# Kernel optimization log

Hardware: AMD Instinct MI355X
Metric: run time of the kernel (lower is better)

Reference implementation:

```python
import jax, jax.numpy as jnp
import numpy as np

# Sizes
N = 4096        # nodes
E = 32768       # edges
NEF = 128       # n_edge_features
HID = 128       # hidden_features
MUL0 = 64       # multiplicity of 0e irreps
MUL1 = 16       # multiplicity of 1o irreps
DIM = MUL0 + 3 * MUL1  # 112
# e3nn FullyConnectedTensorProduct('64x0e+16x1o', '1x0e+1x1o', '64x0e+16x1o')
# instruction order (i_in1, i_in2, i_out): (0,0,0),(0,1,1),(1,0,1),(1,1,0)
WN_A = MUL0 * MUL0   # 0e x 0e -> 0e : 4096
WN_B = MUL0 * MUL1   # 0e x 1o -> 1o : 1024
WN_C = MUL1 * MUL1   # 1o x 0e -> 1o : 256
WN_D = MUL1 * MUL0   # 1o x 1o -> 0e : 1024
WNUM = WN_A + WN_B + WN_C + WN_D  # 6400
# path normalization (irrep_normalization='component', path_normalization='element'):
# alpha = dim(ir_out) / sum_{paths into same output}(mul1*mul2)
N0 = float(np.sqrt(1.0 / (MUL0 + MUL1)))       # scalar output: 1/sqrt(80)
N1 = float(np.sqrt(3.0 / (MUL0 + MUL1)))       # vector output: sqrt(3/80)
INV_SQRT3 = float(1.0 / np.sqrt(3.0))          # wigner-3j factor for l=1 paths


def setup_inputs() -> dict:
    key = jax.random.key(0)
    ks = jax.random.split(key, 8)
    node_attr = jax.random.normal(ks[0], (N, DIM), jnp.float32)
    edge_index = jax.random.randint(ks[1], (2, E), 0, N)
    edge_attr = jax.random.normal(ks[2], (E, NEF), jnp.float32)
    edge_sh = jax.random.normal(ks[3], (E, 4), jnp.float32)
    global_graph_embedding = jax.random.normal(ks[4], (8, 1024), jnp.float32)
    ptr = jnp.sort(jax.random.randint(ks[5], (9,), 0, N))
    W1 = jax.random.normal(ks[6], (NEF, HID), jnp.float32) / np.sqrt(NEF)
    b1 = jnp.zeros((HID,), jnp.float32)
    W2 = jax.random.normal(ks[7], (HID, WNUM), jnp.float32) / np.sqrt(HID)
    b2 = jnp.zeros((WNUM,), jnp.float32)
    return dict(node_attr=node_attr, edge_index=edge_index, edge_attr=edge_attr,
                edge_sh=edge_sh, global_graph_embedding=global_graph_embedding,
                ptr=ptr, W1=W1, b1=b1, W2=W2, b2=b2)


def _tp_conv(node_attr, src, dst, edge_attr, edge_sh, W1, b1, W2, b2):
    # edge MLP -> per-edge tensor-product weights
    h = jax.nn.relu(edge_attr @ W1 + b1)
    w = h @ W2 + b2                                   # (E, 6400)
    # gather and split gathered node features into irreps
    x = node_attr[dst]                                # (E, 112)
    s = x[:, :MUL0]                                   # (E, 64) scalars 0e
    v = x[:, MUL0:].reshape(-1, MUL1, 3)              # (E, 16, 3) vectors 1o
    sh0 = edge_sh[:, :1]                              # (E, 1)
    sh1 = edge_sh[:, 1:]                              # (E, 3)
    i = 0
    wA = w[:, i:i + WN_A].reshape(-1, MUL0, MUL0); i += WN_A
    wB = w[:, i:i + WN_B].reshape(-1, MUL0, MUL1); i += WN_B
    wC = w[:, i:i + WN_C].reshape(-1, MUL1, MUL1); i += WN_C
    wD = w[:, i:i + WN_D].reshape(-1, MUL1, MUL0); i += WN_D
    # scalar output channel: 0e*0e->0e  and  1o.1o->0e (dot product CG)
    out0 = N0 * (jnp.einsum('euw,eu->ew', wA, s) * sh0
                 + INV_SQRT3 * jnp.einsum('euw,eui,ei->ew', wD, v, sh1))
    # vector output channel: 0e*1o->1o  and  1o*0e->1o
    out1 = N1 * (INV_SQRT3 * jnp.einsum('euw,eu,ei->ewi', wB, s, sh1)
                 + INV_SQRT3 * jnp.einsum('euw,eui->ewi', wC, v) * sh0[:, :, None])
    tp = jnp.concatenate([out0, out1.reshape(-1, 3 * MUL1)], axis=-1)  # (E, 112)
    # scatter-mean over edge_src (torch_scatter 'mean': empty segments -> 0)
    sums = jax.ops.segment_sum(tp, src, num_segments=N)
    cnt = jax.ops.segment_sum(jnp.ones((tp.shape[0],), tp.dtype), src, num_segments=N)
    return sums / jnp.maximum(cnt, 1.0)[:, None]


def reference(node_attr, edge_index, edge_attr, edge_sh, global_graph_embedding, ptr, W1, b1, W2, b2):
    src, dst = edge_index[0], edge_index[1]
    out = _tp_conv(node_attr, src, dst, edge_attr, edge_sh, W1, b1, W2, b2)
    # add_in=False -> global branch skipped; residual: in/out dims equal so F.pad is identity
    return out + node_attr
```

## Files before the change

kernel.cpp:

```cpp
#include <hip/hip_runtime.h>

typedef unsigned short u16;
typedef __bf16 bf8 __attribute__((ext_vector_type(8)));
typedef float f4 __attribute__((ext_vector_type(4)));

#define E_EDGES 32768
#define N_NODES 4096
#define N0_CONST 0.1118033988749895f
#define INV_SQRT3_CONST 0.5773502691896258f

__device__ __forceinline__ u16 f2bf(float f) {
    unsigned u = __float_as_uint(f);
    u += 0x7FFFu + ((u >> 16) & 1u);
    return (u16)(u >> 16);
}

__global__ __launch_bounds__(256) void k_prep(const float* __restrict__ W2, const float* __restrict__ W1,
                                              const int* __restrict__ edge_index,
                                              u16* __restrict__ w2s, u16* __restrict__ w1t,
                                              int* __restrict__ deg) {
    int b = blockIdx.x;
    int tid = threadIdx.x;
    if (b < 400) {
        int ks = tid >> 6, l = tid & 63;
        int el = l & 15, q4 = l >> 4;
        int c = b * 16 + el;
        u16 tmp[8];
#pragma unroll
        for (int j = 0; j < 8; j++) {
            int k = ks * 32 + q4 * 8 + j;
            tmp[j] = f2bf(W2[(size_t)k * 6400 + c]);
        }
        *(uint4*)(w2s + b * 2048 + ks * 512 + l * 8) = *(uint4*)tmp;
    } else if (b < 416) {
        int t = (b - 400) * 256 + tid;
#pragma unroll
        for (int i = 0; i < 4; i++) {
            int idx = t * 4 + i;
            int c = idx >> 7, k = idx & 127;
            w1t[idx] = f2bf(W1[k * 128 + c]);
        }
    } else {
        int t = (b - 416) * 256 + tid;
        atomicAdd(&deg[edge_index[t]], 1);
    }
}

__global__ void k_scan(const int* __restrict__ deg, int* __restrict__ ptr, int* __restrict__ cursor) {
    int t = threadIdx.x;
    int base = t * 64;
    int s = 0;
    for (int i = 0; i < 64; i++) s += deg[base + i];
    int x = s;
#pragma unroll
    for (int d = 1; d < 64; d <<= 1) {
        int y = __shfl_up(x, d, 64);
        if (t >= d) x += y;
    }
    int run = x - s;
    for (int i = 0; i < 64; i++) {
        ptr[base + i] = run;
        cursor[base + i] = run;
        run += deg[base + i];
    }
    if (t == 63) ptr[4096] = run;
}

__global__ __launch_bounds__(256) void k_h(const float* __restrict__ ea,
                                           const u16* __restrict__ w1t,
                                           const float* __restrict__ b1,
                                           const int* __restrict__ edge_index,
                                           int* __restrict__ cursor,
                                           int* __restrict__ eids,
                                           u16* __restrict__ h) {
    __shared__ alignas(16) u16 ea_s[64][128];
    int tid = threadIdx.x;
    int e0 = blockIdx.x * 64;
    if (tid < 64) {
        int ge = e0 + tid;
        int s = edge_index[ge];
        int pos = atomicAdd(&cursor[s], 1);
        eids[pos] = ge;
    }
    {
        int e = tid >> 2, q = tid & 3;
        const float4* src = (const float4*)(ea + (size_t)(e0 + e) * 128 + q * 32);
#pragma unroll
        for (int i = 0; i < 8; i++) {
            float4 f = src[i];
            int c = q * 32 + i * 4;
            ea_s[e][c + 0] = f2bf(f.x); ea_s[e][c + 1] = f2bf(f.y);
            ea_s[e][c + 2] = f2bf(f.z); ea_s[e][c + 3] = f2bf(f.w);
        }
    }
    __syncthreads();
    int lane = tid & 63, wave = tid >> 6;
    int el = lane & 15, q4 = lane >> 4;
    f4 acc[4][2];
#pragma unroll
    for (int m = 0; m < 4; m++)
#pragma unroll
        for (int nt = 0; nt < 2; nt++) acc[m][nt] = (f4){0.f, 0.f, 0.f, 0.f};
#pragma unroll
    for (int ks = 0; ks < 4; ks++) {
        bf8 a[4], b[2];
#pragma unroll
        for (int m = 0; m < 4; m++) a[m] = *(const bf8*)&ea_s[m * 16 + el][ks * 32 + q4 * 8];
#pragma unroll
        for (int nt = 0; nt < 2; nt++) {
            int n = wave * 32 + nt * 16 + el;
            b[nt] = *(const bf8*)(w1t + n * 128 + ks * 32 + q4 * 8);
        }
#pragma unroll
        for (int m = 0; m < 4; m++)
#pragma unroll
            for (int nt = 0; nt < 2; nt++)
                acc[m][nt] = __builtin_amdgcn_mfma_f32_16x16x32_bf16(a[m], b[nt], acc[m][nt], 0, 0, 0);
    }
#pragma unroll
    for (int m = 0; m < 4; m++)
#pragma unroll
        for (int nt = 0; nt < 2; nt++) {
            int n = wave * 32 + nt * 16 + el;
            float bias = b1[n];
#pragma unroll
            for (int r = 0; r < 4; r++) {
                int e = e0 + m * 16 + q4 * 4 + r;
                float v = fmaxf(acc[m][nt][r] + bias, 0.f);
                h[(size_t)e * 128 + n] = f2bf(v);
            }
        }
}

__global__ __launch_bounds__(256, 2) void k_main(const u16* __restrict__ w2s,
                                                 const u16* __restrict__ hgl,
                                                 const float* __restrict__ b2,
                                                 const float* __restrict__ node_attr,
                                                 const int* __restrict__ edge_index,
                                                 const float* __restrict__ edge_sh,
                                                 float* __restrict__ tp) {
    __shared__ alignas(16) union {
        u16 h[64][136];
        struct { float bcB[64][17]; float bcC[3][64][17]; } bc;
    } ovl;
    __shared__ float sT[64][66];
    __shared__ float vT[3][16][66];
    __shared__ float pT[16][66];
    __shared__ float sh0_s[64];
    __shared__ float sh1_s[3][64];
    __shared__ int dst_s[64];

    int tid = threadIdx.x;
    int e0 = blockIdx.x * 64;
    int lane = tid & 63, wave = tid >> 6;
    int el = lane & 15, q4 = lane >> 4;

    bf8 a0[4], a1[4];
    float4 bb0, bb1;
    auto loadA = [&](int i, bf8 (&a)[4], float4& bb) {
        int g = (i < 20) ? 64 + i : (i < 84 ? i - 20 : i);
        int pn = 4 * g + wave;
        const u16* gp = w2s + (size_t)pn * 2048 + lane * 8;
        a[0] = *(const bf8*)(gp);
        a[1] = *(const bf8*)(gp + 512);
        a[2] = *(const bf8*)(gp + 1024);
        a[3] = *(const bf8*)(gp + 1536);
        bb = *(const float4*)(b2 + pn * 16 + q4 * 4);
    };
    loadA(0, a0, bb0);

    if (tid < 64) {
        int ge = e0 + tid;
        dst_s[tid] = edge_index[E_EDGES + ge];
        float4 sh = *(const float4*)(edge_sh + (size_t)ge * 4);
        sh0_s[tid] = sh.x; sh1_s[0][tid] = sh.y; sh1_s[1][tid] = sh.z; sh1_s[2][tid] = sh.w;
    }
    __syncthreads();

    {
        int e = tid >> 2, q = tid & 3;
        int dst = dst_s[e];
        const float* xp = node_attr + (size_t)dst * 112;
#pragma unroll
        for (int i = 0; i < 4; i++) {
            float4 f = *(const float4*)(xp + q * 16 + i * 4);
            int u = q * 16 + i * 4;
            sT[u + 0][e] = f.x; sT[u + 1][e] = f.y; sT[u + 2][e] = f.z; sT[u + 3][e] = f.w;
        }
        float vv[12];
#pragma unroll
        for (int i = 0; i < 3; i++) {
            float4 f = *(const float4*)(xp + 64 + q * 12 + i * 4);
            vv[i * 4 + 0] = f.x; vv[i * 4 + 1] = f.y; vv[i * 4 + 2] = f.z; vv[i * 4 + 3] = f.w;
        }
        float s1x = sh1_s[0][e], s1y = sh1_s[1][e], s1z = sh1_s[2][e];
#pragma unroll
        for (int u = 0; u < 4; u++) {
            float xa = vv[u * 3 + 0], xb = vv[u * 3 + 1], xc = vv[u * 3 + 2];
            int uu = q * 4 + u;
            vT[0][uu][e] = xa; vT[1][uu][e] = xb; vT[2][uu][e] = xc;
            pT[uu][e] = INV_SQRT3_CONST * (xa * s1x + xb * s1y + xc * s1z);
        }
        const uint4* hsrc = (const uint4*)(hgl + (size_t)(e0 + e) * 128) + q * 4;
        uint4* hdst = (uint4*)(&ovl.h[e][q * 32]);
#pragma unroll
        for (int i = 0; i < 4; i++) hdst[i] = hsrc[i];
    }
    __syncthreads();

    bf8 hbf[4][4];
#pragma unroll
    for (int nt = 0; nt < 4; nt++)
#pragma unroll
        for (int ks = 0; ks < 4; ks++)
            hbf[nt][ks] = *(const bf8*)&ovl.h[nt * 16 + el][ks * 32 + q4 * 8];
    float sh0n4[4];
#pragma unroll
    for (int nt = 0; nt < 4; nt++) sh0n4[nt] = sh0_s[nt * 16 + el];
    __syncthreads();

    for (int idx = tid; idx < 4352; idx += 256) ((float*)&ovl.bc)[idx] = 0.f;
    __syncthreads();

    auto mfmaG = [&](const bf8 (&a)[4], const float4& bb, f4 (&wf)[4]) {
#pragma unroll
        for (int nt = 0; nt < 4; nt++) wf[nt] = (f4){bb.x, bb.y, bb.z, bb.w};
#pragma unroll
        for (int ks = 0; ks < 4; ks++)
#pragma unroll
            for (int nt = 0; nt < 4; nt++)
                wf[nt] = __builtin_amdgcn_mfma_f32_16x16x32_bf16(a[ks], hbf[nt][ks], wf[nt], 0, 0, 0);
    };

#define STEP(INXT, ACUR, BBCUR, ANXT, BBNXT, CON) \
    { if ((INXT) < 100) loadA((INXT), ANXT, BBNXT); mfmaG(ACUR, BBCUR, wf); CON; }

    f4 wf[4];

    {
        f4 accBn[4];
#pragma unroll
        for (int nt = 0; nt < 4; nt++) accBn[nt] = (f4){0.f, 0.f, 0.f, 0.f};
        auto conB = [&](int ib) {
            int u = 4 * ib + wave;
#pragma unroll
            for (int nt = 0; nt < 4; nt++) {
                float f = sT[u][nt * 16 + el];
                accBn[nt] += f * wf[nt];
            }
        };
        for (int ii = 0; ii < 16; ii += 2) {
            STEP(ii + 1, a0, bb0, a1, bb1, conB(ii));
            STEP(ii + 2, a1, bb1, a0, bb0, conB(ii + 1));
        }
#pragma unroll
        for (int nt = 0; nt < 4; nt++)
#pragma unroll
            for (int r = 0; r < 4; r++)
                atomicAdd(&ovl.bc.bcB[nt * 16 + el][q4 * 4 + r], accBn[nt][r]);
    }

    {
        f4 accCn[3][4];
#pragma unroll
        for (int i3 = 0; i3 < 3; i3++)
#pragma unroll
            for (int nt = 0; nt < 4; nt++) accCn[i3][nt] = (f4){0.f, 0.f, 0.f, 0.f};
        auto conC = [&](int ic) {
            int u = 4 * ic + wave;
#pragma unroll
            for (int nt = 0; nt < 4; nt++) {
#pragma unroll
                for (int i3 = 0; i3 < 3; i3++) {
                    float f = vT[i3][u][nt * 16 + el];
                    accCn[i3][nt] += f * wf[nt];
                }
            }
        };
        for (int ii = 0; ii < 4; ii += 2) {
            STEP(16 + ii + 1, a0, bb0, a1, bb1, conC(ii));
            STEP(16 + ii + 2, a1, bb1, a0, bb0, conC(ii + 1));
        }
#pragma unroll
        for (int i3 = 0; i3 < 3; i3++)
#pragma unroll
            for (int nt = 0; nt < 4; nt++)
#pragma unroll
                for (int r = 0; r < 4; r++)
                    atomicAdd(&ovl.bc.bcC[i3][nt * 16 + el][q4 * 4 + r], accCn[i3][nt][r]);
    }

    f4 acc0n[4];
#pragma unroll
    for (int nt = 0; nt < 4; nt++) acc0n[nt] = (f4){0.f, 0.f, 0.f, 0.f};
    {
        auto conA = [&](int ia) {
#pragma unroll
            for (int nt = 0; nt < 4; nt++) {
                float f = sh0n4[nt] * sT[ia][nt * 16 + el];
                acc0n[nt] += f * wf[nt];
            }
        };
        for (int ii = 0; ii < 64; ii += 2) {
            STEP(20 + ii + 1, a0, bb0, a1, bb1, conA(ii));
            STEP(20 + ii + 2, a1, bb1, a0, bb0, conA(ii + 1));
        }
        auto conD = [&](int id_) {
#pragma unroll
            for (int nt = 0; nt < 4; nt++) {
                float f = pT[id_][nt * 16 + el];
                acc0n[nt] += f * wf[nt];
            }
        };
        for (int ii = 0; ii < 16; ii += 2) {
            STEP(84 + ii + 1, a0, bb0, a1, bb1, conD(ii));
            STEP(84 + ii + 2, a1, bb1, a0, bb0, conD(ii + 1));
        }
    }
#undef STEP

    __syncthreads();

#pragma unroll
    for (int nt = 0; nt < 4; nt++)
#pragma unroll
        for (int r = 0; r < 4; r++)
            sT[nt * 16 + el][wave * 16 + q4 * 4 + r] = N0_CONST * acc0n[nt][r];
    {
        float* vflat = (float*)vT;
        for (int idx = tid; idx < 3072; idx += 256) {
            int e = idx / 48;
            int rem = idx - e * 48;
            int w = rem / 3;
            int i3 = rem - w * 3;
            vflat[idx] = N0_CONST * (ovl.bc.bcB[e][w] * sh1_s[i3][e] + ovl.bc.bcC[i3][e][w] * sh0_s[e]);
        }
    }
    __syncthreads();

    {
        const float* vflat = (const float*)vT;
        float* tpe = tp + (size_t)e0 * 112;
        for (int idx = tid; idx < 64 * 112; idx += 256) {
            int e = idx / 112;
            int c = idx - e * 112;
            float val = (c < 64) ? sT[e][c] : vflat[e * 48 + (c - 64)];
            __builtin_nontemporal_store(val, &tpe[idx]);
        }
    }
}

__global__ __launch_bounds__(128) void k_red(const float* __restrict__ tp,
                                             const int* __restrict__ ptr,
                                             const int* __restrict__ eids,
                                             const float* __restrict__ node_attr,
                                             float* __restrict__ out) {
    int n = blockIdx.x;
    int c = threadIdx.x;
    if (c >= 112) return;
    int a = ptr[n], b = ptr[n + 1];
    float s = 0.f;
    for (int i = a; i < b; i++) {
        int e = eids[i];
        s += tp[(size_t)e * 112 + c];
    }
    float d = fmaxf((float)(b - a), 1.f);
    out[n * 112 + c] = s / d + node_attr[n * 112 + c];
}

extern "C" void kernel_launch(void* const* d_in, const int* in_sizes, int n_in,
                              void* d_out, int out_size, void* d_ws, size_t ws_size,
                              hipStream_t stream) {
    const float* node_attr  = (const float*)d_in[0];
    const int*   edge_index = (const int*)d_in[1];
    const float* edge_attr  = (const float*)d_in[2];
    const float* edge_sh    = (const float*)d_in[3];
    const float* W1         = (const float*)d_in[6];
    const float* b1         = (const float*)d_in[7];
    const float* W2         = (const float*)d_in[8];
    const float* b2         = (const float*)d_in[9];
    float* out = (float*)d_out;

    char* ws = (char*)d_ws;
    u16*   w2s    = (u16*)ws;
    u16*   w1t    = (u16*)(ws + 1638400);
    u16*   hgl    = (u16*)(ws + 1671168);
    float* tp     = (float*)(ws + 10059776);
    int*   deg    = (int*)(ws + 24739840);
    int*   ptr    = (int*)(ws + 24756224);
    int*   cursor = (int*)(ws + 24772624);
    int*   eids   = (int*)(ws + 24789024);

    hipMemsetAsync(deg, 0, 16384, stream);
    k_prep<<<544, 256, 0, stream>>>(W2, W1, edge_index, w2s, w1t, deg);
    k_scan<<<1, 64, 0, stream>>>(deg, ptr, cursor);
    k_h<<<512, 256, 0, stream>>>(edge_attr, w1t, b1, edge_index, cursor, eids, hgl);
    k_main<<<512, 256, 0, stream>>>(w2s, hgl, b2, node_attr, edge_index, edge_sh, tp);
    k_red<<<4096, 128, 0, stream>>>(tp, ptr, eids, node_attr, out);
}
```

Before: 196.3 us.

## Split k_main MFMA K-dimension across two wave halves with 512-thread blocks

Doubles k_main blocks to 512 threads and splits the 128-wide hidden K dimension between two groups of four waves, so each wave holds half the A and B fragments and issues half the MFMAs per step. Partial sums are combined through shared-memory atomics (now issued per step for the C path) and a second-phase add into sT for the scalar outputs. The aim is more waves per CU to hide W2 load latency and lower register pressure. The cost is extra LDS atomics, an extra barrier, and duplicated contraction work, since both halves run the FMA contraction on their own partial weights.

```diff
diff --git a/kernel.cpp b/kernel.cpp
--- a/kernel.cpp
+++ b/kernel.cpp
@@ -132,7 +132,7 @@
         }
 }
 
-__global__ __launch_bounds__(256, 2) void k_main(const u16* __restrict__ w2s,
+__global__ __launch_bounds__(512, 4) void k_main(const u16* __restrict__ w2s,
                                                  const u16* __restrict__ hgl,
                                                  const float* __restrict__ b2,
                                                  const float* __restrict__ node_attr,
@@ -153,19 +153,19 @@
     int tid = threadIdx.x;
     int e0 = blockIdx.x * 64;
     int lane = tid & 63, wave = tid >> 6;
+    int tl = wave & 3, half = wave >> 2;
     int el = lane & 15, q4 = lane >> 4;
 
-    bf8 a0[4], a1[4];
+    bf8 a0[2], a1[2];
     float4 bb0, bb1;
-    auto loadA = [&](int i, bf8 (&a)[4], float4& bb) {
+    auto loadA = [&](int i, bf8 (&a)[2], float4& bb) {
         int g = (i < 20) ? 64 + i : (i < 84 ? i - 20 : i);
-        int pn = 4 * g + wave;
-        const u16* gp = w2s + (size_t)pn * 2048 + lane * 8;
+        int pn = 4 * g + tl;
+        const u16* gp = w2s + (size_t)pn * 2048 + half * 1024 + lane * 8;
         a[0] = *(const bf8*)(gp);
         a[1] = *(const bf8*)(gp + 512);
-        a[2] = *(const bf8*)(gp + 1024);
-        a[3] = *(const bf8*)(gp + 1536);
-        bb = *(const float4*)(b2 + pn * 16 + q4 * 4);
+        bb = (half == 0) ? *(const float4*)(b2 + pn * 16 + q4 * 4)
+                         : (float4){0.f, 0.f, 0.f, 0.f};
     };
     loadA(0, a0, bb0);
 
@@ -177,7 +177,7 @@
     }
     __syncthreads();
 
-    {
+    if (tid < 256) {
         int e = tid >> 2, q = tid & 3;
         int dst = dst_s[e];
         const float* xp = node_attr + (size_t)dst * 112;
@@ -208,25 +208,25 @@
     }
     __syncthreads();
 
-    bf8 hbf[4][4];
+    bf8 hbf[4][2];
 #pragma unroll
     for (int nt = 0; nt < 4; nt++)
 #pragma unroll
-        for (int ks = 0; ks < 4; ks++)
-            hbf[nt][ks] = *(const bf8*)&ovl.h[nt * 16 + el][ks * 32 + q4 * 8];
+        for (int ks = 0; ks < 2; ks++)
+            hbf[nt][ks] = *(const bf8*)&ovl.h[nt * 16 + el][half * 64 + ks * 32 + q4 * 8];
     float sh0n4[4];
 #pragma unroll
     for (int nt = 0; nt < 4; nt++) sh0n4[nt] = sh0_s[nt * 16 + el];
     __syncthreads();
 
-    for (int idx = tid; idx < 4352; idx += 256) ((float*)&ovl.bc)[idx] = 0.f;
-    __syncthreads();
-
-    auto mfmaG = [&](const bf8 (&a)[4], const float4& bb, f4 (&wf)[4]) {
+    for (int idx = tid; idx < 4352; idx += 512) ((float*)&ovl.bc)[idx] = 0.f;
+    __syncthreads();
+
+    auto mfmaG = [&](const bf8 (&a)[2], const float4& bb, f4 (&wf)[4]) {
 #pragma unroll
         for (int nt = 0; nt < 4; nt++) wf[nt] = (f4){bb.x, bb.y, bb.z, bb.w};
 #pragma unroll
-        for (int ks = 0; ks < 4; ks++)
+        for (int ks = 0; ks < 2; ks++)
 #pragma unroll
             for (int nt = 0; nt < 4; nt++)
                 wf[nt] = __builtin_amdgcn_mfma_f32_16x16x32_bf16(a[ks], hbf[nt][ks], wf[nt], 0, 0, 0);
@@ -242,7 +242,7 @@
 #pragma unroll
         for (int nt = 0; nt < 4; nt++) accBn[nt] = (f4){0.f, 0.f, 0.f, 0.f};
         auto conB = [&](int ib) {
-            int u = 4 * ib + wave;
+            int u = 4 * ib + tl;
 #pragma unroll
             for (int nt = 0; nt < 4; nt++) {
                 float f = sT[u][nt * 16 + el];
@@ -261,19 +261,17 @@
     }
 
     {
-        f4 accCn[3][4];
-#pragma unroll
-        for (int i3 = 0; i3 < 3; i3++)
-#pragma unroll
-            for (int nt = 0; nt < 4; nt++) accCn[i3][nt] = (f4){0.f, 0.f, 0.f, 0.f};
         auto conC = [&](int ic) {
-            int u = 4 * ic + wave;
+            int u = 4 * ic + tl;
 #pragma unroll
             for (int nt = 0; nt < 4; nt++) {
 #pragma unroll
                 for (int i3 = 0; i3 < 3; i3++) {
                     float f = vT[i3][u][nt * 16 + el];
-                    accCn[i3][nt] += f * wf[nt];
+                    f4 t = f * wf[nt];
+#pragma unroll
+                    for (int r = 0; r < 4; r++)
+                        atomicAdd(&ovl.bc.bcC[i3][nt * 16 + el][q4 * 4 + r], t[r]);
                 }
             }
         };
@@ -281,13 +279,6 @@
             STEP(16 + ii + 1, a0, bb0, a1, bb1, conC(ii));
             STEP(16 + ii + 2, a1, bb1, a0, bb0, conC(ii + 1));
         }
-#pragma unroll
-        for (int i3 = 0; i3 < 3; i3++)
-#pragma unroll
-            for (int nt = 0; nt < 4; nt++)
-#pragma unroll
-                for (int r = 0; r < 4; r++)
-                    atomicAdd(&ovl.bc.bcC[i3][nt * 16 + el][q4 * 4 + r], accCn[i3][nt][r]);
     }
 
     f4 acc0n[4];
@@ -321,14 +312,16 @@
 
     __syncthreads();
 
-#pragma unroll
-    for (int nt = 0; nt < 4; nt++)
-#pragma unroll
-        for (int r = 0; r < 4; r++)
-            sT[nt * 16 + el][wave * 16 + q4 * 4 + r] = N0_CONST * acc0n[nt][r];
+    if (half == 0) {
+#pragma unroll
+        for (int nt = 0; nt < 4; nt++)
+#pragma unroll
+            for (int r = 0; r < 4; r++)
+                sT[nt * 16 + el][tl * 16 + q4 * 4 + r] = N0_CONST * acc0n[nt][r];
+    }
     {
         float* vflat = (float*)vT;
-        for (int idx = tid; idx < 3072; idx += 256) {
+        for (int idx = tid; idx < 3072; idx += 512) {
             int e = idx / 48;
             int rem = idx - e * 48;
             int w = rem / 3;
@@ -337,11 +330,19 @@
         }
     }
     __syncthreads();
+    if (half == 1) {
+#pragma unroll
+        for (int nt = 0; nt < 4; nt++)
+#pragma unroll
+            for (int r = 0; r < 4; r++)
+                sT[nt * 16 + el][tl * 16 + q4 * 4 + r] += N0_CONST * acc0n[nt][r];
+    }
+    __syncthreads();
 
     {
         const float* vflat = (const float*)vT;
         float* tpe = tp + (size_t)e0 * 112;
-        for (int idx = tid; idx < 64 * 112; idx += 256) {
+        for (int idx = tid; idx < 64 * 112; idx += 512) {
             int e = idx / 112;
             int c = idx - e * 112;
             float val = (c < 64) ? sT[e][c] : vflat[e * 48 + (c - 64)];
@@ -395,6 +396,6 @@
     k_prep<<<544, 256, 0, stream>>>(W2, W1, edge_index, w2s, w1t, deg);
     k_scan<<<1, 64, 0, stream>>>(deg, ptr, cursor);
     k_h<<<512, 256, 0, stream>>>(edge_attr, w1t, b1, edge_index, cursor, eids, hgl);
-    k_main<<<512, 256, 0, stream>>>(w2s, hgl, b2, node_attr, edge_index, edge_sh, tp);
+    k_main<<<512, 512, 0, stream>>>(w2s, hgl, b2, node_attr, edge_index, edge_sh, tp);
     k_red<<<4096, 128, 0, stream>>>(tp, ptr, eids, node_attr, out);
 }
```

New measurement: 560.5 us. 2.86x slower.

## Halve edges per k_main block to raise occupancy and stage W2 transpose via LDS

Applied to the files above, without the earlier changes.

k_main now handles 32 edges per block instead of 64. This shrinks the register accumulators and shared-memory tiles, doubles the grid to 1024 blocks, and raises the launch-bounds occupancy hint from 2 to 4 blocks per CU. In exchange, each block streams the full set of W2 A-fragments for half as many edges, so W2 weight traffic per edge doubles. Separately, k_prep reads W2 rows coalesced into a padded shared tile before converting to bf16, replacing strided global reads.

```diff
diff --git a/kernel.cpp b/kernel.cpp
--- a/kernel.cpp
+++ b/kernel.cpp
@@ -22,15 +22,23 @@
     int b = blockIdx.x;
     int tid = threadIdx.x;
     if (b < 400) {
+        __shared__ float w2l[128][17];
+        {
+            int k = tid >> 1, c8 = (tid & 1) * 8;
+            const float* src = W2 + (size_t)k * 6400 + b * 16 + c8;
+            float tmpf[8];
+#pragma unroll
+            for (int j = 0; j < 8; j++) tmpf[j] = src[j];
+#pragma unroll
+            for (int j = 0; j < 8; j++) w2l[k][c8 + j] = tmpf[j];
+        }
+        __syncthreads();
         int ks = tid >> 6, l = tid & 63;
         int el = l & 15, q4 = l >> 4;
-        int c = b * 16 + el;
         u16 tmp[8];
 #pragma unroll
-        for (int j = 0; j < 8; j++) {
-            int k = ks * 32 + q4 * 8 + j;
-            tmp[j] = f2bf(W2[(size_t)k * 6400 + c]);
-        }
+        for (int j = 0; j < 8; j++)
+            tmp[j] = f2bf(w2l[ks * 32 + q4 * 8 + j][el]);
         *(uint4*)(w2s + b * 2048 + ks * 512 + l * 8) = *(uint4*)tmp;
     } else if (b < 416) {
         int t = (b - 400) * 256 + tid;
@@ -132,7 +140,7 @@
         }
 }
 
-__global__ __launch_bounds__(256, 2) void k_main(const u16* __restrict__ w2s,
+__global__ __launch_bounds__(256, 4) void k_main(const u16* __restrict__ w2s,
                                                  const u16* __restrict__ hgl,
                                                  const float* __restrict__ b2,
                                                  const float* __restrict__ node_attr,
@@ -140,18 +148,18 @@
                                                  const float* __restrict__ edge_sh,
                                                  float* __restrict__ tp) {
     __shared__ alignas(16) union {
-        u16 h[64][136];
-        struct { float bcB[64][17]; float bcC[3][64][17]; } bc;
+        u16 h[32][136];
+        struct { float bcB[32][17]; float bcC[3][32][17]; } bc;
     } ovl;
-    __shared__ float sT[64][66];
-    __shared__ float vT[3][16][66];
-    __shared__ float pT[16][66];
-    __shared__ float sh0_s[64];
-    __shared__ float sh1_s[3][64];
-    __shared__ int dst_s[64];
+    __shared__ float sT[64][34];
+    __shared__ float vT[3][16][34];
+    __shared__ float pT[16][34];
+    __shared__ float sh0_s[32];
+    __shared__ float sh1_s[3][32];
+    __shared__ int dst_s[32];
 
     int tid = threadIdx.x;
-    int e0 = blockIdx.x * 64;
+    int e0 = blockIdx.x * 32;
     int lane = tid & 63, wave = tid >> 6;
     int el = lane & 15, q4 = lane >> 4;
 
@@ -169,7 +177,7 @@
     };
     loadA(0, a0, bb0);
 
-    if (tid < 64) {
+    if (tid < 32) {
         int ge = e0 + tid;
         dst_s[tid] = edge_index[E_EDGES + ge];
         float4 sh = *(const float4*)(edge_sh + (size_t)ge * 4);
@@ -178,73 +186,77 @@
     __syncthreads();
 
     {
-        int e = tid >> 2, q = tid & 3;
-        int dst = dst_s[e];
-        const float* xp = node_attr + (size_t)dst * 112;
-#pragma unroll
-        for (int i = 0; i < 4; i++) {
-            float4 f = *(const float4*)(xp + q * 16 + i * 4);
-            int u = q * 16 + i * 4;
-            sT[u + 0][e] = f.x; sT[u + 1][e] = f.y; sT[u + 2][e] = f.z; sT[u + 3][e] = f.w;
-        }
-        float vv[12];
-#pragma unroll
-        for (int i = 0; i < 3; i++) {
-            float4 f = *(const float4*)(xp + 64 + q * 12 + i * 4);
-            vv[i * 4 + 0] = f.x; vv[i * 4 + 1] = f.y; vv[i * 4 + 2] = f.z; vv[i * 4 + 3] = f.w;
-        }
-        float s1x = sh1_s[0][e], s1y = sh1_s[1][e], s1z = sh1_s[2][e];
-#pragma unroll
-        for (int u = 0; u < 4; u++) {
-            float xa = vv[u * 3 + 0], xb = vv[u * 3 + 1], xc = vv[u * 3 + 2];
-            int uu = q * 4 + u;
-            vT[0][uu][e] = xa; vT[1][uu][e] = xb; vT[2][uu][e] = xc;
-            pT[uu][e] = INV_SQRT3_CONST * (xa * s1x + xb * s1y + xc * s1z);
-        }
-        const uint4* hsrc = (const uint4*)(hgl + (size_t)(e0 + e) * 128) + q * 4;
-        uint4* hdst = (uint4*)(&ovl.h[e][q * 32]);
-#pragma unroll
-        for (int i = 0; i < 4; i++) hdst[i] = hsrc[i];
-    }
-    __syncthreads();
-
-    bf8 hbf[4][4];
-#pragma unroll
-    for (int nt = 0; nt < 4; nt++)
+        int e = tid >> 3, q = tid & 7;
+        if (q < 4) {
+            int dst = dst_s[e];
+            const float* xp = node_attr + (size_t)dst * 112;
+#pragma unroll
+            for (int i = 0; i < 4; i++) {
+                float4 f = *(const float4*)(xp + q * 16 + i * 4);
+                int u = q * 16 + i * 4;
+                sT[u + 0][e] = f.x; sT[u + 1][e] = f.y; sT[u + 2][e] = f.z; sT[u + 3][e] = f.w;
+            }
+            float vv[12];
+#pragma unroll
+            for (int i = 0; i < 3; i++) {
+                float4 f = *(const float4*)(xp + 64 + q * 12 + i * 4);
+                vv[i * 4 + 0] = f.x; vv[i * 4 + 1] = f.y; vv[i * 4 + 2] = f.z; vv[i * 4 + 3] = f.w;
+            }
+            float s1x = sh1_s[0][e], s1y = sh1_s[1][e], s1z = sh1_s[2][e];
+#pragma unroll
+            for (int u = 0; u < 4; u++) {
+                float xa = vv[u * 3 + 0], xb = vv[u * 3 + 1], xc = vv[u * 3 + 2];
+                int uu = q * 4 + u;
+                vT[0][uu][e] = xa; vT[1][uu][e] = xb; vT[2][uu][e] = xc;
+                pT[uu][e] = INV_SQRT3_CONST * (xa * s1x + xb * s1y + xc * s1z);
+            }
+        } else {
+            int qq = q - 4;
+            const uint4* hsrc = (const uint4*)(hgl + (size_t)(e0 + e) * 128) + qq * 4;
+            uint4* hdst = (uint4*)(&ovl.h[e][qq * 32]);
+#pragma unroll
+            for (int i = 0; i < 4; i++) hdst[i] = hsrc[i];
+        }
+    }
+    __syncthreads();
+
+    bf8 hbf[2][4];
+#pragma unroll
+    for (int nt = 0; nt < 2; nt++)
 #pragma unroll
         for (int ks = 0; ks < 4; ks++)
             hbf[nt][ks] = *(const bf8*)&ovl.h[nt * 16 + el][ks * 32 + q4 * 8];
-    float sh0n4[4];
-#pragma unroll
-    for (int nt = 0; nt < 4; nt++) sh0n4[nt] = sh0_s[nt * 16 + el];
-    __syncthreads();
-
-    for (int idx = tid; idx < 4352; idx += 256) ((float*)&ovl.bc)[idx] = 0.f;
-    __syncthreads();
-
-    auto mfmaG = [&](const bf8 (&a)[4], const float4& bb, f4 (&wf)[4]) {
-#pragma unroll
-        for (int nt = 0; nt < 4; nt++) wf[nt] = (f4){bb.x, bb.y, bb.z, bb.w};
+    float sh0n2[2];
+#pragma unroll
+    for (int nt = 0; nt < 2; nt++) sh0n2[nt] = sh0_s[nt * 16 + el];
+    __syncthreads();
+
+    for (int idx = tid; idx < 2176; idx += 256) ((float*)&ovl.bc)[idx] = 0.f;
+    __syncthreads();
+
+    auto mfmaG = [&](const bf8 (&a)[4], const float4& bb, f4 (&wf)[2]) {
+#pragma unroll
+        for (int nt = 0; nt < 2; nt++) wf[nt] = (f4){bb.x, bb.y, bb.z, bb.w};
 #pragma unroll
         for (int ks = 0; ks < 4; ks++)
 #pragma unroll
-            for (int nt = 0; nt < 4; nt++)
+            for (int nt = 0; nt < 2; nt++)
                 wf[nt] = __builtin_amdgcn_mfma_f32_16x16x32_bf16(a[ks], hbf[nt][ks], wf[nt], 0, 0, 0);
     };
 
 #define STEP(INXT, ACUR, BBCUR, ANXT, BBNXT, CON) \
     { if ((INXT) < 100) loadA((INXT), ANXT, BBNXT); mfmaG(ACUR, BBCUR, wf); CON; }
 
-    f4 wf[4];
-
-    {
-        f4 accBn[4];
-#pragma unroll
-        for (int nt = 0; nt < 4; nt++) accBn[nt] = (f4){0.f, 0.f, 0.f, 0.f};
+    f4 wf[2];
+
+    {
+        f4 accBn[2];
+#pragma unroll
+        for (int nt = 0; nt < 2; nt++) accBn[nt] = (f4){0.f, 0.f, 0.f, 0.f};
         auto conB = [&](int ib) {
             int u = 4 * ib + wave;
 #pragma unroll
-            for (int nt = 0; nt < 4; nt++) {
+            for (int nt = 0; nt < 2; nt++) {
                 float f = sT[u][nt * 16 + el];
                 accBn[nt] += f * wf[nt];
             }
@@ -254,22 +266,22 @@
             STEP(ii + 2, a1, bb1, a0, bb0, conB(ii + 1));
         }
 #pragma unroll
-        for (int nt = 0; nt < 4; nt++)
+        for (int nt = 0; nt < 2; nt++)
 #pragma unroll
             for (int r = 0; r < 4; r++)
                 atomicAdd(&ovl.bc.bcB[nt * 16 + el][q4 * 4 + r], accBn[nt][r]);
     }
 
     {
-        f4 accCn[3][4];
+        f4 accCn[3][2];
 #pragma unroll
         for (int i3 = 0; i3 < 3; i3++)
 #pragma unroll
-            for (int nt = 0; nt < 4; nt++) accCn[i3][nt] = (f4){0.f, 0.f, 0.f, 0.f};
+            for (int nt = 0; nt < 2; nt++) accCn[i3][nt] = (f4){0.f, 0.f, 0.f, 0.f};
         auto conC = [&](int ic) {
             int u = 4 * ic + wave;
 #pragma unroll
-            for (int nt = 0; nt < 4; nt++) {
+            for (int nt = 0; nt < 2; nt++) {
 #pragma unroll
                 for (int i3 = 0; i3 < 3; i3++) {
                     float f = vT[i3][u][nt * 16 + el];
@@ -284,20 +296,20 @@
 #pragma unroll
         for (int i3 = 0; i3 < 3; i3++)
 #pragma unroll
-            for (int nt = 0; nt < 4; nt++)
+            for (int nt = 0; nt < 2; nt++)
 #pragma unroll
                 for (int r = 0; r < 4; r++)
                     atomicAdd(&ovl.bc.bcC[i3][nt * 16 + el][q4 * 4 + r], accCn[i3][nt][r]);
     }
 
-    f4 acc0n[4];
-#pragma unroll
-    for (int nt = 0; nt < 4; nt++) acc0n[nt] = (f4){0.f, 0.f, 0.f, 0.f};
+    f4 acc0n[2];
+#pragma unroll
+    for (int nt = 0; nt < 2; nt++) acc0n[nt] = (f4){0.f, 0.f, 0.f, 0.f};
     {
         auto conA = [&](int ia) {
 #pragma unroll
-            for (int nt = 0; nt < 4; nt++) {
-                float f = sh0n4[nt] * sT[ia][nt * 16 + el];
+            for (int nt = 0; nt < 2; nt++) {
+                float f = sh0n2[nt] * sT[ia][nt * 16 + el];
                 acc0n[nt] += f * wf[nt];
             }
         };
@@ -307,7 +319,7 @@
         }
         auto conD = [&](int id_) {
 #pragma unroll
-            for (int nt = 0; nt < 4; nt++) {
+            for (int nt = 0; nt < 2; nt++) {
                 float f = pT[id_][nt * 16 + el];
                 acc0n[nt] += f * wf[nt];
             }
@@ -321,14 +333,17 @@
 
     __syncthreads();
 
-#pragma unroll
-    for (int nt = 0; nt < 4; nt++)
-#pragma unroll
-        for (int r = 0; r < 4; r++)
-            sT[nt * 16 + el][wave * 16 + q4 * 4 + r] = N0_CONST * acc0n[nt][r];
+    {
+        float* out0 = (float*)sT;
+#pragma unroll
+        for (int nt = 0; nt < 2; nt++)
+#pragma unroll
+            for (int r = 0; r < 4; r++)
+                out0[(nt * 16 + el) * 64 + wave * 16 + q4 * 4 + r] = N0_CONST * acc0n[nt][r];
+    }
     {
         float* vflat = (float*)vT;
-        for (int idx = tid; idx < 3072; idx += 256) {
+        for (int idx = tid; idx < 1536; idx += 256) {
             int e = idx / 48;
             int rem = idx - e * 48;
             int w = rem / 3;
@@ -339,12 +354,13 @@
     __syncthreads();
 
     {
+        const float* out0 = (const float*)sT;
         const float* vflat = (const float*)vT;
         float* tpe = tp + (size_t)e0 * 112;
-        for (int idx = tid; idx < 64 * 112; idx += 256) {
+        for (int idx = tid; idx < 32 * 112; idx += 256) {
             int e = idx / 112;
             int c = idx - e * 112;
-            float val = (c < 64) ? sT[e][c] : vflat[e * 48 + (c - 64)];
+            float val = (c < 64) ? out0[e * 64 + c] : vflat[e * 48 + (c - 64)];
             __builtin_nontemporal_store(val, &tpe[idx]);
         }
     }
@@ -395,6 +411,6 @@
     k_prep<<<544, 256, 0, stream>>>(W2, W1, edge_index, w2s, w1t, deg);
     k_scan<<<1, 64, 0, stream>>>(deg, ptr, cursor);
     k_h<<<512, 256, 0, stream>>>(edge_attr, w1t, b1, edge_index, cursor, eids, hgl);
-    k_main<<<512, 256, 0, stream>>>(w2s, hgl, b2, node_attr, edge_index, edge_sh, tp);
+    k_main<<<1024, 256, 0, stream>>>(w2s, hgl, b2, node_attr, edge_index, edge_sh, tp);
     k_red<<<4096, 128, 0, stream>>>(tp, ptr, eids, node_attr, out);
 }
```

After: 209.5 us. +6.8%, slower.

## Replace CSR scatter-mean with atomic accumulation and stage W2 transpose via LDS

Applied to the files above, without the earlier changes.

Removes the scan kernel, the per-edge sort into CSR buckets and the tp intermediate buffer. k_main now atomically adds each edge's tensor-product output into the zero-initialised output, and a small finalize kernel divides by degree and adds the residual. The W2 bf16 repack also stages a tile through shared memory so the global reads coalesce. The trade is about 3.7M float atomics with contention on popular nodes, and a summation order that is no longer deterministic.

```diff
diff --git a/kernel.cpp b/kernel.cpp
--- a/kernel.cpp
+++ b/kernel.cpp
@@ -22,15 +22,23 @@
     int b = blockIdx.x;
     int tid = threadIdx.x;
     if (b < 400) {
+        __shared__ float w2l[128][17];
+        {
+            int k = tid >> 1, c8 = (tid & 1) * 8;
+            const float* src = W2 + (size_t)k * 6400 + b * 16 + c8;
+            float tmpf[8];
+#pragma unroll
+            for (int j = 0; j < 8; j++) tmpf[j] = src[j];
+#pragma unroll
+            for (int j = 0; j < 8; j++) w2l[k][c8 + j] = tmpf[j];
+        }
+        __syncthreads();
         int ks = tid >> 6, l = tid & 63;
         int el = l & 15, q4 = l >> 4;
-        int c = b * 16 + el;
         u16 tmp[8];
 #pragma unroll
-        for (int j = 0; j < 8; j++) {
-            int k = ks * 32 + q4 * 8 + j;
-            tmp[j] = f2bf(W2[(size_t)k * 6400 + c]);
-        }
+        for (int j = 0; j < 8; j++)
+            tmp[j] = f2bf(w2l[ks * 32 + q4 * 8 + j][el]);
         *(uint4*)(w2s + b * 2048 + ks * 512 + l * 8) = *(uint4*)tmp;
     } else if (b < 416) {
         int t = (b - 400) * 256 + tid;
@@ -46,42 +54,13 @@
     }
 }
 
-__global__ void k_scan(const int* __restrict__ deg, int* __restrict__ ptr, int* __restrict__ cursor) {
-    int t = threadIdx.x;
-    int base = t * 64;
-    int s = 0;
-    for (int i = 0; i < 64; i++) s += deg[base + i];
-    int x = s;
-#pragma unroll
-    for (int d = 1; d < 64; d <<= 1) {
-        int y = __shfl_up(x, d, 64);
-        if (t >= d) x += y;
-    }
-    int run = x - s;
-    for (int i = 0; i < 64; i++) {
-        ptr[base + i] = run;
-        cursor[base + i] = run;
-        run += deg[base + i];
-    }
-    if (t == 63) ptr[4096] = run;
-}
-
 __global__ __launch_bounds__(256) void k_h(const float* __restrict__ ea,
                                            const u16* __restrict__ w1t,
                                            const float* __restrict__ b1,
-                                           const int* __restrict__ edge_index,
-                                           int* __restrict__ cursor,
-                                           int* __restrict__ eids,
                                            u16* __restrict__ h) {
     __shared__ alignas(16) u16 ea_s[64][128];
     int tid = threadIdx.x;
     int e0 = blockIdx.x * 64;
-    if (tid < 64) {
-        int ge = e0 + tid;
-        int s = edge_index[ge];
-        int pos = atomicAdd(&cursor[s], 1);
-        eids[pos] = ge;
-    }
     {
         int e = tid >> 2, q = tid & 3;
         const float4* src = (const float4*)(ea + (size_t)(e0 + e) * 128 + q * 32);
@@ -138,7 +117,7 @@
                                                  const float* __restrict__ node_attr,
                                                  const int* __restrict__ edge_index,
                                                  const float* __restrict__ edge_sh,
-                                                 float* __restrict__ tp) {
+                                                 float* __restrict__ outsum) {
     __shared__ alignas(16) union {
         u16 h[64][136];
         struct { float bcB[64][17]; float bcC[3][64][17]; } bc;
@@ -149,6 +128,7 @@
     __shared__ float sh0_s[64];
     __shared__ float sh1_s[3][64];
     __shared__ int dst_s[64];
+    __shared__ int src_s[64];
 
     int tid = threadIdx.x;
     int e0 = blockIdx.x * 64;
@@ -171,6 +151,7 @@
 
     if (tid < 64) {
         int ge = e0 + tid;
+        src_s[tid] = edge_index[ge];
         dst_s[tid] = edge_index[E_EDGES + ge];
         float4 sh = *(const float4*)(edge_sh + (size_t)ge * 4);
         sh0_s[tid] = sh.x; sh1_s[0][tid] = sh.y; sh1_s[1][tid] = sh.z; sh1_s[2][tid] = sh.w;
@@ -340,32 +321,23 @@
 
     {
         const float* vflat = (const float*)vT;
-        float* tpe = tp + (size_t)e0 * 112;
         for (int idx = tid; idx < 64 * 112; idx += 256) {
             int e = idx / 112;
             int c = idx - e * 112;
             float val = (c < 64) ? sT[e][c] : vflat[e * 48 + (c - 64)];
-            __builtin_nontemporal_store(val, &tpe[idx]);
-        }
-    }
-}
-
-__global__ __launch_bounds__(128) void k_red(const float* __restrict__ tp,
-                                             const int* __restrict__ ptr,
-                                             const int* __restrict__ eids,
+            atomicAdd(&outsum[(size_t)src_s[e] * 112 + c], val);
+        }
+    }
+}
+
+__global__ __launch_bounds__(128) void k_fin(const int* __restrict__ deg,
                                              const float* __restrict__ node_attr,
                                              float* __restrict__ out) {
     int n = blockIdx.x;
     int c = threadIdx.x;
     if (c >= 112) return;
-    int a = ptr[n], b = ptr[n + 1];
-    float s = 0.f;
-    for (int i = a; i < b; i++) {
-        int e = eids[i];
-        s += tp[(size_t)e * 112 + c];
-    }
-    float d = fmaxf((float)(b - a), 1.f);
-    out[n * 112 + c] = s / d + node_attr[n * 112 + c];
+    float d = fmaxf((float)deg[n], 1.f);
+    out[n * 112 + c] = out[n * 112 + c] / d + node_attr[n * 112 + c];
 }
 
 extern "C" void kernel_launch(void* const* d_in, const int* in_sizes, int n_in,
@@ -385,16 +357,12 @@
     u16*   w2s    = (u16*)ws;
     u16*   w1t    = (u16*)(ws + 1638400);
     u16*   hgl    = (u16*)(ws + 1671168);
-    float* tp     = (float*)(ws + 10059776);
-    int*   deg    = (int*)(ws + 24739840);
-    int*   ptr    = (int*)(ws + 24756224);
-    int*   cursor = (int*)(ws + 24772624);
-    int*   eids   = (int*)(ws + 24789024);
+    int*   deg    = (int*)(ws + 10059776);
 
     hipMemsetAsync(deg, 0, 16384, stream);
+    hipMemsetAsync(out, 0, (size_t)N_NODES * 112 * 4, stream);
     k_prep<<<544, 256, 0, stream>>>(W2, W1, edge_index, w2s, w1t, deg);
-    k_scan<<<1, 64, 0, stream>>>(deg, ptr, cursor);
-    k_h<<<512, 256, 0, stream>>>(edge_attr, w1t, b1, edge_index, cursor, eids, hgl);
-    k_main<<<512, 256, 0, stream>>>(w2s, hgl, b2, node_attr, edge_index, edge_sh, tp);
-    k_red<<<4096, 128, 0, stream>>>(tp, ptr, eids, node_attr, out);
-}
+    k_h<<<512, 256, 0, stream>>>(edge_attr, w1t, b1, hgl);
+    k_main<<<512, 256, 0, stream>>>(w2s, hgl, b2, node_attr, edge_index, edge_sh, out);
+    k_fin<<<4096, 128, 0, stream>>>(deg, node_attr, out);
+}
```

New measurement: 189.5 us. 3.4% less time.
